# Optimization experiments

Measured on AMD Instinct MI355X. Metric: run time of the kernel, lower is better.

Reference implementation:

```python
import jax, jax.numpy as jnp
import numpy as np

B, T, N, C_IN = 64, 48, 1000, 2
H = 64            # hidden_dim
EMB = 16          # emb_dim
HORIZON = 12
C_OUT = 1


def setup_inputs() -> dict:
    key = jax.random.key(0)
    ks = jax.random.split(key, 16)
    nrm = lambda k, shp, s: (jax.random.normal(k, shp, dtype=jnp.float32) * s)
    return {
        'x':   nrm(ks[0], (B, T, N, C_IN), 1.0),
        'E1':  nrm(ks[1], (N, EMB), 0.1),
        'E2':  nrm(ks[2], (N, EMB), 0.1),
        # layer 0: gc_x Linear(C_IN -> 4H), gc_h Linear(H -> 4H); torch weight layout [out,in]
        'Wx0': nrm(ks[3], (4 * H, C_IN), 0.05), 'bx0': jnp.zeros((4 * H,), jnp.float32),
        'Wh0': nrm(ks[4], (4 * H, H), 0.05),    'bh0': jnp.zeros((4 * H,), jnp.float32),
        # layer 1: gc_x Linear(H -> 4H), gc_h Linear(H -> 4H)
        'Wx1': nrm(ks[5], (4 * H, H), 0.05),    'bx1': jnp.zeros((4 * H,), jnp.float32),
        'Wh1': nrm(ks[6], (4 * H, H), 0.05),    'bh1': jnp.zeros((4 * H,), jnp.float32),
        # proj: Linear(H -> C_OUT * HORIZON)
        'Wp':  nrm(ks[7], (C_OUT * HORIZON, H), 0.05), 'bp': jnp.zeros((C_OUT * HORIZON,), jnp.float32),
    }


def _cell(xt, h_prev, c_prev, A, Wx, bx, Wh, bh):
    # gates = lin(A @ xt) + lin(A @ h_prev)   -> [B,N,4H]
    gates = (jnp.einsum('ij,bjc->bic', A, xt) @ Wx.T + bx
             + jnp.einsum('ij,bjh->bih', A, h_prev) @ Wh.T + bh)
    i, f, o, g = jnp.split(gates, 4, axis=-1)
    i, f, o = jax.nn.sigmoid(i), jax.nn.sigmoid(f), jax.nn.sigmoid(o)
    g = jnp.tanh(g)
    c_t = f * c_prev + i * g
    h_t = o * jnp.tanh(c_t)
    return h_t, c_t


def reference(x, E1, E2, Wx0, bx0, Wh0, bh0, Wx1, bx1, Wh1, bh1, Wp, bp):
    A = jax.nn.softmax(jax.nn.relu(E1 @ E2.T), axis=-1)  # [N,N]
    b = x.shape[0]
    zeros = jnp.zeros((b, N, H), x.dtype)

    def step(carry, xt):
        h0, c0, h1, c1 = carry
        h0, c0 = _cell(xt, h0, c0, A, Wx0, bx0, Wh0, bh0)
        h1, c1 = _cell(h0, h1, c1, A, Wx1, bx1, Wh1, bh1)
        return (h0, c0, h1, c1), None

    xs = jnp.transpose(x, (1, 0, 2, 3))  # [T,B,N,C]
    (h0, c0, h1, c1), _ = jax.lax.scan(step, (zeros, zeros, zeros, zeros), xs)
    out = h1 @ Wp.T + bp                              # [B,N,HORIZON*C_OUT]
    out = out.reshape(b, N, HORIZON, -1)
    return jnp.transpose(out, (0, 2, 1, 3))           # [B,HORIZON,N,C_OUT]
```

## Files before the change

### kernel.cpp

```cpp
#include <hip/hip_runtime.h>
#include <math.h>

typedef float f4 __attribute__((ext_vector_type(4)));
typedef _Float16 h4 __attribute__((ext_vector_type(4)));
typedef _Float16 h8 __attribute__((ext_vector_type(8)));

#define WS_AX    0
#define WS_AHC   6144000
#define WS_C0    14532608
#define WS_C1    18628608
#define WS_HTH   22724608
#define WS_HTL   26918912
#define WS_A16H  31113216
#define WS_A16L  31637504
#define WS_W0T   32161792
#define WS_W1T   32178176

__global__ __launch_bounds__(256) void compute_A(const float* __restrict__ E1,
                                                 const float* __restrict__ E2,
                                                 float* __restrict__ At)
{
    __shared__ double z[1000];
    __shared__ double red[256];
    __shared__ double e1[16];
    const int i = blockIdx.x;
    const int tid = threadIdx.x;
    if (tid < 16) e1[tid] = (double)E1[i * 16 + tid];
    __syncthreads();
    double lmax = -1e300;
    for (int j = tid; j < 1000; j += 256) {
        double s = 0.0;
        #pragma unroll
        for (int c = 0; c < 16; ++c) s += e1[c] * (double)E2[j * 16 + c];
        if (s < 0.0) s = 0.0;
        z[j] = s;
        if (s > lmax) lmax = s;
    }
    red[tid] = lmax; __syncthreads();
    for (int off = 128; off > 0; off >>= 1) {
        if (tid < off) red[tid] = fmax(red[tid], red[tid + off]);
        __syncthreads();
    }
    const double zmax = red[0];
    __syncthreads();
    double lsum = 0.0;
    for (int j = tid; j < 1000; j += 256) {
        double e = exp(z[j] - zmax);
        z[j] = e;
        lsum += e;
    }
    red[tid] = lsum; __syncthreads();
    for (int off = 128; off > 0; off >>= 1) {
        if (tid < off) red[tid] += red[tid + off];
        __syncthreads();
    }
    const double inv = 1.0 / red[0];
    for (int j = tid; j < 1000; j += 256)
        At[(size_t)j * 1000 + i] = (float)(z[j] * inv);
}

__global__ __launch_bounds__(256) void transpose_x(const float* __restrict__ x,
                                                   float* __restrict__ Xr)
{
    int o = blockIdx.x * 256 + threadIdx.x;
    if (o >= 6144000) return;
    int j = o / 6144;
    int r = o - j * 6144;
    int t = r >> 7;
    int q = r & 127;
    int b = q >> 1;
    int c = q & 1;
    Xr[o] = x[(((size_t)(b * 48 + t)) * 1000 + j) * 2 + c];
}

__global__ __launch_bounds__(256) void zero_kernel(float* __restrict__ p, int n4)
{
    int i = blockIdx.x * 256 + threadIdx.x;
    if (i < n4) { f4 z = {0.f, 0.f, 0.f, 0.f}; ((f4*)p)[i] = z; }
}

__global__ __launch_bounds__(256) void prep_w(const float* __restrict__ Wh0,
                                              const float* __restrict__ Wx1,
                                              const float* __restrict__ Wh1,
                                              float* __restrict__ W0T,
                                              float* __restrict__ W1T)
{
    int idx = blockIdx.x * 256 + threadIdx.x;
    if (idx < 16384) {
        int k = idx >> 8, o = idx & 255;
        W0T[idx] = Wh0[o * 64 + k];
    }
    int j = idx - 16384;
    if (j >= 0 && j < 32768) {
        int k = j >> 8, o = j & 255;
        W1T[j] = (k < 64) ? Wx1[o * 64 + k] : Wh1[o * 64 + (k - 64)];
    }
}

__global__ __launch_bounds__(256) void prep_A(const float* __restrict__ At,
                                              _Float16* __restrict__ Ahh,
                                              _Float16* __restrict__ All)
{
    int idx = blockIdx.x * 256 + threadIdx.x;
    int m = idx >> 10, k = idx & 1023;
    float v = (m < 1000 && k < 1000) ? At[(size_t)k * 1000 + m] : 0.f;
    _Float16 hi = (_Float16)v;
    Ahh[idx] = hi;
    All[idx] = (_Float16)((v - (float)hi) * 2048.f);
}

__global__ __launch_bounds__(256) void gemm1000(const float* __restrict__ At,
                                                const float* __restrict__ B,
                                                float* __restrict__ C,
                                                int ncols)
{
    __shared__ float As[8][64];
    __shared__ float Bs[8][128];
    const int tid = threadIdx.x;
    const int tx = tid & 15;
    const int ty = tid >> 4;
    const int row0 = blockIdx.x * 64;
    const int col0 = blockIdx.y * 128;
    const int lm = tid & 63;
    const int lk = tid >> 6;
    const int bcol = tid & 127;
    const int bk = tid >> 7;
    const bool arow_ok = (row0 + lm) < 1000;

    float acc[4][8];
    #pragma unroll
    for (int r = 0; r < 4; ++r)
        #pragma unroll
        for (int c = 0; c < 8; ++c) acc[r][c] = 0.f;

    for (int k0 = 0; k0 < 1000; k0 += 8) {
        float a0 = arow_ok ? At[(size_t)(k0 + lk) * 1000 + row0 + lm] : 0.f;
        float a1 = arow_ok ? At[(size_t)(k0 + lk + 4) * 1000 + row0 + lm] : 0.f;
        float bv[4];
        #pragma unroll
        for (int kk = 0; kk < 4; ++kk)
            bv[kk] = B[(size_t)(k0 + bk * 4 + kk) * ncols + col0 + bcol];
        __syncthreads();
        As[lk][lm] = a0;
        As[lk + 4][lm] = a1;
        #pragma unroll
        for (int kk = 0; kk < 4; ++kk) Bs[bk * 4 + kk][bcol] = bv[kk];
        __syncthreads();
        #pragma unroll
        for (int k = 0; k < 8; ++k) {
            f4 av = *(const f4*)&As[k][ty * 4];
            f4 b0 = *(const f4*)&Bs[k][tx * 8];
            f4 b1 = *(const f4*)&Bs[k][tx * 8 + 4];
            #pragma unroll
            for (int r = 0; r < 4; ++r) {
                float a = av[r];
                acc[r][0] = fmaf(a, b0[0], acc[r][0]);
                acc[r][1] = fmaf(a, b0[1], acc[r][1]);
                acc[r][2] = fmaf(a, b0[2], acc[r][2]);
                acc[r][3] = fmaf(a, b0[3], acc[r][3]);
                acc[r][4] = fmaf(a, b1[0], acc[r][4]);
                acc[r][5] = fmaf(a, b1[1], acc[r][5]);
                acc[r][6] = fmaf(a, b1[2], acc[r][6]);
                acc[r][7] = fmaf(a, b1[3], acc[r][7]);
            }
        }
    }
    #pragma unroll
    for (int r = 0; r < 4; ++r) {
        int row = row0 + ty * 4 + r;
        if (row < 1000) {
            f4 o0 = {acc[r][0], acc[r][1], acc[r][2], acc[r][3]};
            f4 o1 = {acc[r][4], acc[r][5], acc[r][6], acc[r][7]};
            *(f4*)&C[(size_t)row * ncols + col0 + tx * 8]     = o0;
            *(f4*)&C[(size_t)row * ncols + col0 + tx * 8 + 4] = o1;
        }
    }
}

#define GL16(srcp, dstoff) \
    __builtin_amdgcn_global_load_lds((const __attribute__((address_space(1))) unsigned int*)(srcp), \
        (__attribute__((address_space(3))) unsigned int*)(lds + (dstoff)), 16, 0, 0)

__device__ __forceinline__ int swzb(int row, int lg) {
    return row * 64 + ((lg ^ ((row ^ (row >> 2)) & 3)) << 4);
}

__global__ __launch_bounds__(256, 2) void gemm_m(
    const _Float16* __restrict__ Ahg, const _Float16* __restrict__ Alg,
    const _Float16* __restrict__ Bhg, const _Float16* __restrict__ Blg,
    float* __restrict__ Cout)
{
    __shared__ __align__(1024) char lds[24576];
    const int tid = threadIdx.x;
    const int lane = tid & 63;
    const int w = tid >> 6;
    const int lg = lane >> 4, l15 = lane & 15;
    const int m0 = (blockIdx.x & 15) * 64;
    const int n0 = (blockIdx.x >> 4) * 128;

    const int r16 = lane >> 2;
    const int sd = lane & 3;
    const char* src[6];
    #pragma unroll
    for (int q = 0; q < 6; ++q) {
        const int c = w * 6 + q;
        int row;
        const _Float16* g;
        if (c < 4)       { row = (c)      * 16 + r16; g = Ahg + (size_t)(m0 + row) * 1024; }
        else if (c < 8)  { row = (c - 4)  * 16 + r16; g = Alg + (size_t)(m0 + row) * 1024; }
        else if (c < 16) { row = (c - 8)  * 16 + r16; g = Bhg + (size_t)(n0 + row) * 1024; }
        else             { row = (c - 16) * 16 + r16; g = Blg + (size_t)(n0 + row) * 1024; }
        const int cg = sd ^ ((row ^ (row >> 2)) & 3);
        src[q] = (const char*)(g + cg * 8);
    }

    f4 acc0[4][2], acc1[4][2];
    #pragma unroll
    for (int a = 0; a < 4; ++a)
        #pragma unroll
        for (int b = 0; b < 2; ++b) {
            acc0[a][b] = (f4){0.f, 0.f, 0.f, 0.f};
            acc1[a][b] = (f4){0.f, 0.f, 0.f, 0.f};
        }

    for (int ks = 0; ks < 32; ++ks) {
        const int kadv = ks * 64;
        #pragma unroll
        for (int q = 0; q < 6; ++q)
            GL16(src[q] + kadv, (w * 6 + q) * 1024);
        __syncthreads();

        h8 fa[4], fl[4], bh[2], bl[2];
        #pragma unroll
        for (int mf = 0; mf < 4; ++mf) {
            const int ob = swzb(mf * 16 + l15, lg);
            fa[mf] = *(const h8*)(lds + ob);
            fl[mf] = *(const h8*)(lds + 4096 + ob);
        }
        #pragma unroll
        for (int nf = 0; nf < 2; ++nf) {
            const int ob = swzb(w * 32 + nf * 16 + l15, lg);
            bh[nf] = *(const h8*)(lds + 8192 + ob);
            bl[nf] = *(const h8*)(lds + 16384 + ob);
        }
        __syncthreads();

        #pragma unroll
        for (int nf = 0; nf < 2; ++nf)
            #pragma unroll
            for (int mf = 0; mf < 4; ++mf) {
                acc0[mf][nf] = __builtin_amdgcn_mfma_f32_16x16x32_f16(fa[mf], bh[nf], acc0[mf][nf], 0, 0, 0);
                acc1[mf][nf] = __builtin_amdgcn_mfma_f32_16x16x32_f16(fa[mf], bl[nf], acc1[mf][nf], 0, 0, 0);
                acc1[mf][nf] = __builtin_amdgcn_mfma_f32_16x16x32_f16(fl[mf], bh[nf], acc1[mf][nf], 0, 0, 0);
            }
    }

    #pragma unroll
    for (int mf = 0; mf < 4; ++mf)
        #pragma unroll
        for (int nf = 0; nf < 2; ++nf) {
            const int row = m0 + mf * 16 + lg * 4;
            const int col = n0 + w * 32 + nf * 16 + l15;
            #pragma unroll
            for (int e = 0; e < 4; ++e)
                Cout[(size_t)(row + e) * 8192 + col] =
                    acc0[mf][nf][e] + acc1[mf][nf][e] * (1.f / 2048.f);
        }
}

__global__ __launch_bounds__(256) void gates_f(
    const float* __restrict__ AHC, int two,
    const float* __restrict__ WT,
    const float* __restrict__ b1, const float* __restrict__ b2,
    const float* __restrict__ AX, const float* __restrict__ WxE, int t,
    float* __restrict__ Cst,
    _Float16* __restrict__ HTh, _Float16* __restrict__ HTl, int nbase)
{
    __shared__ __align__(16) char smem[43136];
    float (*As)[65] = (float(*)[65])smem;
    float *Bs       = (float*)(smem + 8320);
    float *wx       = (float*)(smem + 41088);
    _Float16 (*Sh)[80] = (_Float16(*)[80])smem;
    _Float16 (*Sl)[80] = (_Float16(*)[80])(smem + 10240);
    const int tid = threadIdx.x;
    const int tx = tid & 15;
    const int ty = tid >> 4;
    const int i0 = (blockIdx.x >> 6) * 64;
    const int b  = blockIdx.x & 63;
    const int mrow = tid >> 3;
    const int f4i  = tid & 7;

    if (WxE && tid < 128) ((f4*)wx)[tid] = ((const f4*)WxE)[tid];

    f4 acc[4][4];
    #pragma unroll
    for (int r = 0; r < 4; ++r)
        #pragma unroll
        for (int gq = 0; gq < 4; ++gq) acc[r][gq] = (f4){0.f, 0.f, 0.f, 0.f};

    const int nchunk = two ? 4 : 2;
    for (int ch = 0; ch < nchunk; ++ch) {
        const int coff = ((ch < 2) ? 0 : 4096) + b * 64;
        const int koff = (ch & 1) * 32;
        f4 av0 = *(const f4*)&AHC[(size_t)(i0 + mrow) * 8192 + coff + koff + f4i * 4];
        f4 av1 = *(const f4*)&AHC[(size_t)(i0 + mrow + 32) * 8192 + coff + koff + f4i * 4];
        const float* wsrc = WT + ch * 8192;
        f4 bv[8];
        #pragma unroll
        for (int r = 0; r < 8; ++r) bv[r] = *(const f4*)&wsrc[(tid + r * 256) * 4];
        __syncthreads();
        #pragma unroll
        for (int j = 0; j < 4; ++j) {
            As[f4i * 4 + j][mrow]      = av0[j];
            As[f4i * 4 + j][mrow + 32] = av1[j];
        }
        #pragma unroll
        for (int r = 0; r < 8; ++r) *(f4*)&Bs[(tid + r * 256) * 4] = bv[r];
        __syncthreads();
        #pragma unroll
        for (int k = 0; k < 32; ++k) {
            float a[4];
            #pragma unroll
            for (int rr = 0; rr < 4; ++rr) a[rr] = As[k][ty * 4 + rr];
            f4 bq[4];
            #pragma unroll
            for (int gq = 0; gq < 4; ++gq) bq[gq] = *(const f4*)&Bs[k * 256 + gq * 64 + tx * 4];
            #pragma unroll
            for (int rr = 0; rr < 4; ++rr)
                #pragma unroll
                for (int gq = 0; gq < 4; ++gq)
                    acc[rr][gq] += a[rr] * bq[gq];
        }
    }

    f4 bb[4];
    #pragma unroll
    for (int gq = 0; gq < 4; ++gq) {
        f4 v1 = *(const f4*)&b1[gq * 64 + tx * 4];
        f4 v2 = *(const f4*)&b2[gq * 64 + tx * 4];
        bb[gq] = v1 + v2;
    }

    f4 hreg[4];
    #pragma unroll
    for (int rr = 0; rr < 4; ++rr) {
        const int i = i0 + ty * 4 + rr;
        const bool valid = (i < 1000);
        f4 gv[4];
        #pragma unroll
        for (int gq = 0; gq < 4; ++gq) gv[gq] = acc[rr][gq] + bb[gq];
        if (WxE && valid) {
            float x0 = AX[(size_t)i * 6144 + t * 128 + b * 2 + 0];
            float x1 = AX[(size_t)i * 6144 + t * 128 + b * 2 + 1];
            #pragma unroll
            for (int gq = 0; gq < 4; ++gq)
                #pragma unroll
                for (int hh = 0; hh < 4; ++hh) {
                    int gc = gq * 64 + tx * 4 + hh;
                    gv[gq][hh] = fmaf(x0, wx[gc * 2 + 0],
                                 fmaf(x1, wx[gc * 2 + 1], gv[gq][hh]));
                }
        }
        f4 hnew = {0.f, 0.f, 0.f, 0.f};
        if (valid) {
            const size_t base = ((size_t)b * 1000 + i) * 64 + tx * 4;
            f4 cold = *(const f4*)&Cst[base];
            f4 cnew;
            #pragma unroll
            for (int hh = 0; hh < 4; ++hh) {
                float ig = 1.f / (1.f + expf(-gv[0][hh]));
                float fg = 1.f / (1.f + expf(-gv[1][hh]));
                float og = 1.f / (1.f + expf(-gv[2][hh]));
                float gg = tanhf(gv[3][hh]);
                float c  = fg * cold[hh] + ig * gg;
                cnew[hh] = c;
                hnew[hh] = og * tanhf(c);
            }
            *(f4*)&Cst[base] = cnew;
        }
        hreg[rr] = hnew;
    }

    __syncthreads();
    #pragma unroll
    for (int hh = 0; hh < 4; ++hh) {
        h4 vh, vl;
        #pragma unroll
        for (int rr = 0; rr < 4; ++rr) {
            float v = hreg[rr][hh];
            _Float16 hi = (_Float16)v;
            vh[rr] = hi;
            vl[rr] = (_Float16)((v - (float)hi) * 2048.f);
        }
        *(h4*)&Sh[tx * 4 + hh][ty * 4] = vh;
        *(h4*)&Sl[tx * 4 + hh][ty * 4] = vl;
    }
    __syncthreads();
    #pragma unroll
    for (int pass = 0; pass < 2; ++pass) {
        const int c = pass * 256 + tid;
        const int row = c >> 3;
        const int off = (c & 7) * 8;
        const size_t go = (size_t)(nbase + b * 64 + row) * 1024 + i0 + off;
        *(h8*)&HTh[go] = *(const h8*)&Sh[row][off];
        *(h8*)&HTl[go] = *(const h8*)&Sl[row][off];
    }
}

__global__ __launch_bounds__(256) void proj_f16(const _Float16* __restrict__ HTh,
                                                const _Float16* __restrict__ HTl,
                                                const float* __restrict__ Wpj,
                                                const float* __restrict__ bp,
                                                float* __restrict__ out)
{
    int i = blockIdx.x * 256 + threadIdx.x;
    if (i >= 1000) return;
    int b = blockIdx.y;
    float hv[64];
    #pragma unroll
    for (int h = 0; h < 64; ++h) {
        size_t o = (size_t)(4096 + b * 64 + h) * 1024 + i;
        hv[h] = (float)HTh[o] + (float)HTl[o] * (1.f / 2048.f);
    }
    #pragma unroll
    for (int hor = 0; hor < 12; ++hor) {
        float s = bp[hor];
        #pragma unroll
        for (int h = 0; h < 64; ++h) s = fmaf(hv[h], Wpj[hor * 64 + h], s);
        out[(size_t)(b * 12 + hor) * 1000 + i] = s;
    }
}

extern "C" void kernel_launch(void* const* d_in, const int* in_sizes, int n_in,
                              void* d_out, int out_size, void* d_ws, size_t ws_size,
                              hipStream_t stream)
{
    const float* x   = (const float*)d_in[0];
    const float* E1  = (const float*)d_in[1];
    const float* E2  = (const float*)d_in[2];
    const float* Wx0 = (const float*)d_in[3];
    const float* bx0 = (const float*)d_in[4];
    const float* Wh0 = (const float*)d_in[5];
    const float* bh0 = (const float*)d_in[6];
    const float* Wx1 = (const float*)d_in[7];
    const float* bx1 = (const float*)d_in[8];
    const float* Wh1 = (const float*)d_in[9];
    const float* bh1 = (const float*)d_in[10];
    const float* Wp  = (const float*)d_in[11];
    const float* bp  = (const float*)d_in[12];
    float* out = (float*)d_out;
    float* ws  = (float*)d_ws;

    float*    AX  = ws + WS_AX;
    float*    AHC = ws + WS_AHC;
    float*    C0  = ws + WS_C0;
    float*    C1  = ws + WS_C1;
    _Float16* HTh = (_Float16*)(ws + WS_HTH);
    _Float16* HTl = (_Float16*)(ws + WS_HTL);
    _Float16* Ah  = (_Float16*)(ws + WS_A16H);
    _Float16* Al  = (_Float16*)(ws + WS_A16L);
    float*    W0T = ws + WS_W0T;
    float*    W1T = ws + WS_W1T;
    float*    At  = ws + WS_C0;
    float*    Xr  = ws + WS_AHC;

    compute_A<<<1000, 256, 0, stream>>>(E1, E2, At);
    transpose_x<<<24000, 256, 0, stream>>>(x, Xr);
    gemm1000<<<dim3(16, 48), 256, 0, stream>>>(At, Xr, AX, 6144);
    prep_w<<<192, 256, 0, stream>>>(Wh0, Wx1, Wh1, W0T, W1T);
    prep_A<<<4096, 256, 0, stream>>>(At, Ah, Al);
    zero_kernel<<<8000, 256, 0, stream>>>(ws + WS_C0, 2048000);
    zero_kernel<<<8192, 256, 0, stream>>>(AHC, 2097152);
    zero_kernel<<<8192, 256, 0, stream>>>(ws + WS_HTH, 2097152);

    for (int t = 0; t < 48; ++t) {
        gates_f<<<1024, 256, 0, stream>>>(AHC, 0, W0T, bh0, bx0,
                                          AX, Wx0, t, C0, HTh, HTl, 0);
        gemm_m<<<1024, 256, 0, stream>>>(Ah, Al, HTh, HTl, AHC);
        gates_f<<<1024, 256, 0, stream>>>(AHC, 1, W1T, bh1, bx1,
                                          nullptr, nullptr, 0, C1, HTh, HTl, 4096);
    }
    proj_f16<<<dim3(4, 64), 256, 0, stream>>>(HTh, HTl, Wp, bp, out);
    (void)in_sizes; (void)n_in; (void)out_size; (void)ws_size;
}
```

Before: 8.483 ms.

## Fuse layer-1 and next-step layer-0 gate kernels and interleave HT per batch

Merges the layer-1 gate update at step t with the layer-0 gate update at step t+1 into one kernel, since both consume the same A@[h0,h1] product, so each timestep needs one gemm plus one gates launch instead of three launches. The HT layout is interleaved per batch (h0 then h1 rows per batch) so a single gemm covers both layers, and the gates kernel writes h4 directly without an LDS transpose. gemm_m block-to-tile mapping is remapped to group N tiles per XCD for cache locality. The last iteration computes a wasted layer-0 step, and the direct uncoalesced h4 stores may cost bandwidth.

```diff
diff --git a/kernel.cpp b/kernel.cpp
--- a/kernel.cpp
+++ b/kernel.cpp
@@ -195,8 +195,10 @@
     const int lane = tid & 63;
     const int w = tid >> 6;
     const int lg = lane >> 4, l15 = lane & 15;
-    const int m0 = (blockIdx.x & 15) * 64;
-    const int n0 = (blockIdx.x >> 4) * 128;
+    const int xcd = blockIdx.x & 7;
+    const int j = blockIdx.x >> 3;
+    const int m0 = (j >> 3) * 64;
+    const int n0 = (xcd * 8 + (j & 7)) * 128;
 
     const int r16 = lane >> 2;
     const int sd = lane & 3;
@@ -268,20 +270,18 @@
         }
 }
 
-__global__ __launch_bounds__(256) void gates_f(
-    const float* __restrict__ AHC, int two,
-    const float* __restrict__ WT,
-    const float* __restrict__ b1, const float* __restrict__ b2,
-    const float* __restrict__ AX, const float* __restrict__ WxE, int t,
-    float* __restrict__ Cst,
-    _Float16* __restrict__ HTh, _Float16* __restrict__ HTl, int nbase)
-{
-    __shared__ __align__(16) char smem[43136];
-    float (*As)[65] = (float(*)[65])smem;
-    float *Bs       = (float*)(smem + 8320);
-    float *wx       = (float*)(smem + 41088);
-    _Float16 (*Sh)[80] = (_Float16(*)[80])smem;
-    _Float16 (*Sl)[80] = (_Float16(*)[80])(smem + 10240);
+__global__ __launch_bounds__(256) void gates_m(
+    const float* __restrict__ AHC, int mode,
+    const float* __restrict__ W1T, const float* __restrict__ W0T,
+    const float* __restrict__ bh1, const float* __restrict__ bx1,
+    const float* __restrict__ bh0, const float* __restrict__ bx0,
+    const float* __restrict__ AX, const float* __restrict__ Wx0E, int t0,
+    float* __restrict__ C1, float* __restrict__ C0,
+    _Float16* __restrict__ HTh, _Float16* __restrict__ HTl)
+{
+    __shared__ float As[32][65];
+    __shared__ float Bs[32 * 256];
+    __shared__ float wx[512];
     const int tid = threadIdx.x;
     const int tx = tid & 15;
     const int ty = tid >> 4;
@@ -290,81 +290,97 @@
     const int mrow = tid >> 3;
     const int f4i  = tid & 7;
 
-    if (WxE && tid < 128) ((f4*)wx)[tid] = ((const f4*)WxE)[tid];
-
-    f4 acc[4][4];
+    if (tid < 128) ((f4*)wx)[tid] = ((const f4*)Wx0E)[tid];
+
+    f4 acc1[4][4], acc0[4][4];
     #pragma unroll
     for (int r = 0; r < 4; ++r)
         #pragma unroll
-        for (int gq = 0; gq < 4; ++gq) acc[r][gq] = (f4){0.f, 0.f, 0.f, 0.f};
-
-    const int nchunk = two ? 4 : 2;
-    for (int ch = 0; ch < nchunk; ++ch) {
-        const int coff = ((ch < 2) ? 0 : 4096) + b * 64;
-        const int koff = (ch & 1) * 32;
-        f4 av0 = *(const f4*)&AHC[(size_t)(i0 + mrow) * 8192 + coff + koff + f4i * 4];
-        f4 av1 = *(const f4*)&AHC[(size_t)(i0 + mrow + 32) * 8192 + coff + koff + f4i * 4];
-        const float* wsrc = WT + ch * 8192;
-        f4 bv[8];
-        #pragma unroll
-        for (int r = 0; r < 8; ++r) bv[r] = *(const f4*)&wsrc[(tid + r * 256) * 4];
-        __syncthreads();
-        #pragma unroll
-        for (int j = 0; j < 4; ++j) {
-            As[f4i * 4 + j][mrow]      = av0[j];
-            As[f4i * 4 + j][mrow + 32] = av1[j];
-        }
-        #pragma unroll
-        for (int r = 0; r < 8; ++r) *(f4*)&Bs[(tid + r * 256) * 4] = bv[r];
-        __syncthreads();
-        #pragma unroll
-        for (int k = 0; k < 32; ++k) {
-            float a[4];
-            #pragma unroll
-            for (int rr = 0; rr < 4; ++rr) a[rr] = As[k][ty * 4 + rr];
-            f4 bq[4];
-            #pragma unroll
-            for (int gq = 0; gq < 4; ++gq) bq[gq] = *(const f4*)&Bs[k * 256 + gq * 64 + tx * 4];
-            #pragma unroll
-            for (int rr = 0; rr < 4; ++rr)
-                #pragma unroll
-                for (int gq = 0; gq < 4; ++gq)
-                    acc[rr][gq] += a[rr] * bq[gq];
-        }
-    }
-
-    f4 bb[4];
+        for (int gq = 0; gq < 4; ++gq) {
+            acc1[r][gq] = (f4){0.f, 0.f, 0.f, 0.f};
+            acc0[r][gq] = (f4){0.f, 0.f, 0.f, 0.f};
+        }
+
+    if (mode) {
+        for (int ch = 0; ch < 4; ++ch) {
+            const int coff = b * 128 + ch * 32;
+            f4 av0 = *(const f4*)&AHC[(size_t)(i0 + mrow) * 8192 + coff + f4i * 4];
+            f4 av1 = *(const f4*)&AHC[(size_t)(i0 + mrow + 32) * 8192 + coff + f4i * 4];
+            const float* wsrc = W1T + ch * 8192;
+            f4 bv[8];
+            #pragma unroll
+            for (int r = 0; r < 8; ++r) bv[r] = *(const f4*)&wsrc[(tid + r * 256) * 4];
+            __syncthreads();
+            #pragma unroll
+            for (int jj = 0; jj < 4; ++jj) {
+                As[f4i * 4 + jj][mrow]      = av0[jj];
+                As[f4i * 4 + jj][mrow + 32] = av1[jj];
+            }
+            #pragma unroll
+            for (int r = 0; r < 8; ++r) *(f4*)&Bs[(tid + r * 256) * 4] = bv[r];
+            __syncthreads();
+            #pragma unroll
+            for (int k = 0; k < 32; ++k) {
+                float a[4];
+                #pragma unroll
+                for (int rr = 0; rr < 4; ++rr) a[rr] = As[k][ty * 4 + rr];
+                f4 bq[4];
+                #pragma unroll
+                for (int gq = 0; gq < 4; ++gq) bq[gq] = *(const f4*)&Bs[k * 256 + gq * 64 + tx * 4];
+                #pragma unroll
+                for (int rr = 0; rr < 4; ++rr)
+                    #pragma unroll
+                    for (int gq = 0; gq < 4; ++gq)
+                        acc1[rr][gq] += a[rr] * bq[gq];
+            }
+            if (ch < 2) {
+                const float* w0src = W0T + ch * 8192;
+                f4 bw[8];
+                #pragma unroll
+                for (int r = 0; r < 8; ++r) bw[r] = *(const f4*)&w0src[(tid + r * 256) * 4];
+                __syncthreads();
+                #pragma unroll
+                for (int r = 0; r < 8; ++r) *(f4*)&Bs[(tid + r * 256) * 4] = bw[r];
+                __syncthreads();
+                #pragma unroll
+                for (int k = 0; k < 32; ++k) {
+                    float a[4];
+                    #pragma unroll
+                    for (int rr = 0; rr < 4; ++rr) a[rr] = As[k][ty * 4 + rr];
+                    f4 bq[4];
+                    #pragma unroll
+                    for (int gq = 0; gq < 4; ++gq) bq[gq] = *(const f4*)&Bs[k * 256 + gq * 64 + tx * 4];
+                    #pragma unroll
+                    for (int rr = 0; rr < 4; ++rr)
+                        #pragma unroll
+                        for (int gq = 0; gq < 4; ++gq)
+                            acc0[rr][gq] += a[rr] * bq[gq];
+                }
+            }
+        }
+    }
+    __syncthreads();
+
+    f4 bb0[4], bb1[4];
     #pragma unroll
     for (int gq = 0; gq < 4; ++gq) {
-        f4 v1 = *(const f4*)&b1[gq * 64 + tx * 4];
-        f4 v2 = *(const f4*)&b2[gq * 64 + tx * 4];
-        bb[gq] = v1 + v2;
-    }
-
-    f4 hreg[4];
+        bb0[gq] = *(const f4*)&bh0[gq * 64 + tx * 4] + *(const f4*)&bx0[gq * 64 + tx * 4];
+        bb1[gq] = *(const f4*)&bh1[gq * 64 + tx * 4] + *(const f4*)&bx1[gq * 64 + tx * 4];
+    }
+
+    f4 h1reg[4], h0reg[4];
     #pragma unroll
     for (int rr = 0; rr < 4; ++rr) {
         const int i = i0 + ty * 4 + rr;
         const bool valid = (i < 1000);
-        f4 gv[4];
-        #pragma unroll
-        for (int gq = 0; gq < 4; ++gq) gv[gq] = acc[rr][gq] + bb[gq];
-        if (WxE && valid) {
-            float x0 = AX[(size_t)i * 6144 + t * 128 + b * 2 + 0];
-            float x1 = AX[(size_t)i * 6144 + t * 128 + b * 2 + 1];
-            #pragma unroll
-            for (int gq = 0; gq < 4; ++gq)
-                #pragma unroll
-                for (int hh = 0; hh < 4; ++hh) {
-                    int gc = gq * 64 + tx * 4 + hh;
-                    gv[gq][hh] = fmaf(x0, wx[gc * 2 + 0],
-                                 fmaf(x1, wx[gc * 2 + 1], gv[gq][hh]));
-                }
-        }
-        f4 hnew = {0.f, 0.f, 0.f, 0.f};
-        if (valid) {
+        f4 h1n = {0.f, 0.f, 0.f, 0.f};
+        f4 h0n = {0.f, 0.f, 0.f, 0.f};
+        if (mode && valid) {
+            f4 gv[4];
+            #pragma unroll
+            for (int gq = 0; gq < 4; ++gq) gv[gq] = acc1[rr][gq] + bb1[gq];
             const size_t base = ((size_t)b * 1000 + i) * 64 + tx * 4;
-            f4 cold = *(const f4*)&Cst[base];
+            f4 cold = *(const f4*)&C1[base];
             f4 cnew;
             #pragma unroll
             for (int hh = 0; hh < 4; ++hh) {
@@ -374,36 +390,63 @@
                 float gg = tanhf(gv[3][hh]);
                 float c  = fg * cold[hh] + ig * gg;
                 cnew[hh] = c;
-                hnew[hh] = og * tanhf(c);
-            }
-            *(f4*)&Cst[base] = cnew;
-        }
-        hreg[rr] = hnew;
-    }
-
-    __syncthreads();
+                h1n[hh] = og * tanhf(c);
+            }
+            *(f4*)&C1[base] = cnew;
+        }
+        if (valid) {
+            f4 gv[4];
+            #pragma unroll
+            for (int gq = 0; gq < 4; ++gq) gv[gq] = acc0[rr][gq] + bb0[gq];
+            float x0 = AX[(size_t)i * 6144 + t0 * 128 + b * 2 + 0];
+            float x1 = AX[(size_t)i * 6144 + t0 * 128 + b * 2 + 1];
+            #pragma unroll
+            for (int gq = 0; gq < 4; ++gq)
+                #pragma unroll
+                for (int hh = 0; hh < 4; ++hh) {
+                    int gc = gq * 64 + tx * 4 + hh;
+                    gv[gq][hh] = fmaf(x0, wx[gc * 2 + 0],
+                                 fmaf(x1, wx[gc * 2 + 1], gv[gq][hh]));
+                }
+            const size_t base = ((size_t)b * 1000 + i) * 64 + tx * 4;
+            f4 cold = *(const f4*)&C0[base];
+            f4 cnew;
+            #pragma unroll
+            for (int hh = 0; hh < 4; ++hh) {
+                float ig = 1.f / (1.f + expf(-gv[0][hh]));
+                float fg = 1.f / (1.f + expf(-gv[1][hh]));
+                float og = 1.f / (1.f + expf(-gv[2][hh]));
+                float gg = tanhf(gv[3][hh]);
+                float c  = fg * cold[hh] + ig * gg;
+                cnew[hh] = c;
+                h0n[hh] = og * tanhf(c);
+            }
+            *(f4*)&C0[base] = cnew;
+        }
+        h1reg[rr] = h1n;
+        h0reg[rr] = h0n;
+    }
+
     #pragma unroll
     for (int hh = 0; hh < 4; ++hh) {
-        h4 vh, vl;
+        h4 vh0, vl0, vh1, vl1;
         #pragma unroll
         for (int rr = 0; rr < 4; ++rr) {
-            float v = hreg[rr][hh];
-            _Float16 hi = (_Float16)v;
-            vh[rr] = hi;
-            vl[rr] = (_Float16)((v - (float)hi) * 2048.f);
-        }
-        *(h4*)&Sh[tx * 4 + hh][ty * 4] = vh;
-        *(h4*)&Sl[tx * 4 + hh][ty * 4] = vl;
-    }
-    __syncthreads();
-    #pragma unroll
-    for (int pass = 0; pass < 2; ++pass) {
-        const int c = pass * 256 + tid;
-        const int row = c >> 3;
-        const int off = (c & 7) * 8;
-        const size_t go = (size_t)(nbase + b * 64 + row) * 1024 + i0 + off;
-        *(h8*)&HTh[go] = *(const h8*)&Sh[row][off];
-        *(h8*)&HTl[go] = *(const h8*)&Sl[row][off];
+            float v0 = h0reg[rr][hh];
+            _Float16 p0 = (_Float16)v0;
+            vh0[rr] = p0; vl0[rr] = (_Float16)((v0 - (float)p0) * 2048.f);
+            float v1 = h1reg[rr][hh];
+            _Float16 p1 = (_Float16)v1;
+            vh1[rr] = p1; vl1[rr] = (_Float16)((v1 - (float)p1) * 2048.f);
+        }
+        const size_t r0 = (size_t)(b * 128 + tx * 4 + hh) * 1024 + i0 + ty * 4;
+        *(h4*)&HTh[r0] = vh0;
+        *(h4*)&HTl[r0] = vl0;
+        if (mode) {
+            const size_t r1 = (size_t)(b * 128 + 64 + tx * 4 + hh) * 1024 + i0 + ty * 4;
+            *(h4*)&HTh[r1] = vh1;
+            *(h4*)&HTl[r1] = vl1;
+        }
     }
 }
 
@@ -419,7 +462,7 @@
     float hv[64];
     #pragma unroll
     for (int h = 0; h < 64; ++h) {
-        size_t o = (size_t)(4096 + b * 64 + h) * 1024 + i;
+        size_t o = (size_t)(b * 128 + 64 + h) * 1024 + i;
         hv[h] = (float)HTh[o] + (float)HTl[o] * (1.f / 2048.f);
     }
     #pragma unroll
@@ -473,12 +516,12 @@
     zero_kernel<<<8192, 256, 0, stream>>>(AHC, 2097152);
     zero_kernel<<<8192, 256, 0, stream>>>(ws + WS_HTH, 2097152);
 
+    gates_m<<<1024, 256, 0, stream>>>(AHC, 0, W1T, W0T, bh1, bx1, bh0, bx0,
+                                      AX, Wx0, 0, C1, C0, HTh, HTl);
     for (int t = 0; t < 48; ++t) {
-        gates_f<<<1024, 256, 0, stream>>>(AHC, 0, W0T, bh0, bx0,
-                                          AX, Wx0, t, C0, HTh, HTl, 0);
         gemm_m<<<1024, 256, 0, stream>>>(Ah, Al, HTh, HTl, AHC);
-        gates_f<<<1024, 256, 0, stream>>>(AHC, 1, W1T, bh1, bx1,
-                                          nullptr, nullptr, 0, C1, HTh, HTl, 4096);
+        gates_m<<<1024, 256, 0, stream>>>(AHC, 1, W1T, W0T, bh1, bx1, bh0, bx0,
+                                          AX, Wx0, (t + 1) & 47, C1, C0, HTh, HTl);
     }
     proj_f16<<<dim3(4, 64), 256, 0, stream>>>(HTh, HTl, Wp, bp, out);
     (void)in_sizes; (void)n_in; (void)out_size; (void)ws_size;
```

Measured after the change: 32.38 ms. 282% more time.
